# Kernel tuning notes

Measured on AMD Instinct MI355X. Metric: run time of the kernel, lower is better.

Reference implementation:

```python
import jax, jax.numpy as jnp
import numpy as np

B, K, L = 8, 288, 16384   # K = C*kh*kw = 32*3*3
O = 64                    # output channels


def setup_inputs() -> dict:
    key = jax.random.key(0)
    k1, k2, k3 = jax.random.split(key, 3)
    x_unf = jax.random.normal(k1, (B, K, L), dtype=jnp.float32)
    w = jax.random.normal(k2, (O, 32, 3, 3), dtype=jnp.float32)
    b = jax.random.normal(k3, (O,), dtype=jnp.float32)
    gamma = jnp.float32(0.005)
    return {"x_unf": x_unf, "w": w, "b": b, "gamma": gamma}


def reference(x_unf, w, b, gamma):
    # torch: l = x_unf.transpose(1,2)[:,:,:,None] - w.view(1,1,-1,w.size(0))
    #        l = sum(l**2, dim=2); t = exp(-gamma*l) + b
    o = w.shape[0]
    wv = jnp.reshape(w, (-1,))            # row-major flatten, same as torch .view
    wv = jnp.reshape(wv, (-1, o))         # [K, O] (memory reinterpretation, NOT transpose)
    xt = jnp.transpose(x_unf, (0, 2, 1))  # [B, L, K]
    x2 = jnp.sum(xt * xt, axis=-1, keepdims=True)       # [B, L, 1]
    w2 = jnp.sum(wv * wv, axis=0)[None, None, :]        # [1, 1, O]
    xw = jnp.einsum('blk,ko->blo', xt, wv)              # [B, L, O]
    d2 = x2 + w2 - 2.0 * xw                             # [B, L, O]
    t = jnp.exp(-gamma * d2)
    return t + b
```

## Files before the change

kernel.cpp:

```cpp
#include <hip/hip_runtime.h>

#define LDIM 16384
#define KDIM 288
#define ODIM 64
#define BDIM 8

typedef float f32x4 __attribute__((ext_vector_type(4)));
typedef short bf16x8 __attribute__((ext_vector_type(8)));

__device__ __forceinline__ short f2bf(float f) {
  unsigned u = __builtin_bit_cast(unsigned, f);
  unsigned r = u + 0x7FFFu + ((u >> 16) & 1u);
  return (short)(r >> 16);
}

__global__ __launch_bounds__(256) void gauss_pre(const float* __restrict__ w,
                                                 const float* __restrict__ gammap,
                                                 short* __restrict__ wfrag,
                                                 float* __restrict__ cw) {
  int tid = threadIdx.x;
  int blk = blockIdx.x;

  if (blk < 9) {
    int kc = blk;
    int ln = tid & 63;
    int nt = tid >> 6;
    int k0 = kc * 32 + (ln >> 4) * 8;
    int n = nt * 16 + (ln & 15);
    bf16x8 v;
#pragma unroll
    for (int j = 0; j < 8; ++j) v[j] = f2bf(w[(k0 + j) * 64 + n]);
    *(bf16x8*)(wfrag + ((kc * 4 + nt) * 64 + ln) * 8) = v;
  } else {
    __shared__ float red[256];
    int o = tid & 63;
    int seg = tid >> 6;
    float s = 0.f;
#pragma unroll 8
    for (int k = seg * 72; k < seg * 72 + 72; ++k) {
      float v = w[k * 64 + o];
      s += v * v;
    }
    red[tid] = s;
    __syncthreads();
    if (tid < 64) {
      float t = red[tid] + red[tid + 64] + red[tid + 128] + red[tid + 192];
      cw[tid] = -gammap[0] * t;
    }
  }
}

__global__ __launch_bounds__(256, 4) void gauss_main(
    const float* __restrict__ x, const short* __restrict__ wfrag,
    const float* __restrict__ cw, const float* __restrict__ bias,
    const float* __restrict__ gammap, float* __restrict__ out) {
  __shared__ float abuf[2][32 * 128];

  const int tid = threadIdx.x;
  const int lane = tid & 63;
  const int wvid = tid >> 6;
  const int m = lane & 15;
  const int quad = lane >> 4;

  const long g0 = (long)blockIdx.x * 128;
  const int bidx = (int)(g0 >> 14);
  const int l0 = (int)(g0 & (LDIM - 1));

  const float* xb = x + (long)bidx * ((long)KDIM * LDIM) + l0;

  const int srow = (lane >> 5);
  const int scolf = (lane & 31) * 4;

#define STAGE(KC, BUF)                                                         \
  {                                                                            \
    const float* xsrc = xb + (long)((KC) * 32) * LDIM;                         \
    _Pragma("unroll") for (int i = 0; i < 4; ++i) {                            \
      int s = wvid * 4 + i;                                                    \
      const float* gp = xsrc + (long)(2 * s + srow) * LDIM + scolf;            \
      __builtin_amdgcn_global_load_lds(                                        \
          (const __attribute__((address_space(1))) unsigned int*)(void*)gp,    \
          (__attribute__((address_space(3))) unsigned int*)&abuf[BUF][s * 256],\
          16, 0, 0);                                                           \
    }                                                                          \
  }

  const f32x4 zero = {0.f, 0.f, 0.f, 0.f};
  f32x4 acc[2][4];
#pragma unroll
  for (int t = 0; t < 2; ++t)
#pragma unroll
    for (int nt = 0; nt < 4; ++nt) acc[t][nt] = zero;
  float s2[2] = {0.f, 0.f};

  STAGE(0, 0)
  STAGE(1, 1)
  __syncthreads();

#pragma unroll 1
  for (int kc = 0; kc < 9; ++kc) {
    const int pb = kc & 1;

    bf16x8 bfr[4];
    const short* wp = wfrag + ((kc * 4) * 64 + lane) * 8;
#pragma unroll
    for (int nt = 0; nt < 4; ++nt) bfr[nt] = *(const bf16x8*)(wp + nt * 512);

#pragma unroll
    for (int t = 0; t < 2; ++t) {
      const float* ap = &abuf[pb][(quad * 8) * 128 + wvid * 32 + t * 16 + m];
      float a[8];
#pragma unroll
      for (int j = 0; j < 8; ++j) a[j] = ap[j * 128];
      bf16x8 afr;
#pragma unroll
      for (int j = 0; j < 8; ++j) {
        s2[t] += a[j] * a[j];
        afr[j] = f2bf(a[j]);
      }
#pragma unroll
      for (int nt = 0; nt < 4; ++nt)
        acc[t][nt] =
            __builtin_amdgcn_mfma_f32_16x16x32_bf16(afr, bfr[nt], acc[t][nt], 0, 0, 0);
    }

    __syncthreads();
    if (kc < 7) STAGE(kc + 2, pb)
  }

#pragma unroll
  for (int t = 0; t < 2; ++t) {
    s2[t] += __shfl_xor(s2[t], 16, 64);
    s2[t] += __shfl_xor(s2[t], 32, 64);
  }

  const float gamma = gammap[0];
  float cwv[4], bv[4];
#pragma unroll
  for (int nt = 0; nt < 4; ++nt) {
    int col = nt * 16 + m;
    cwv[nt] = cw[col];
    bv[nt] = bias[col];
  }

  float* ob = &abuf[0][0] + wvid * 2048;
  const float coef = 2.f * gamma;
#pragma unroll
  for (int t = 0; t < 2; ++t) {
#pragma unroll
    for (int r = 0; r < 4; ++r) {
      int row = quad * 4 + r;
      float x2v = __shfl(s2[t], (lane & 48) | row, 64);
      float cx = -gamma * x2v;
      int lr = t * 16 + row;
#pragma unroll
      for (int nt = 0; nt < 4; ++nt) {
        float e = coef * acc[t][nt][r] + (cx + cwv[nt]);
        ob[lr * 64 + nt * 16 + m] = __expf(e) + bv[nt];
      }
    }
  }
  __syncthreads();

  float* outw = out + (g0 + wvid * 32) * 64;
#pragma unroll
  for (int j = 0; j < 8; ++j) {
    f32x4 v = *(f32x4*)&ob[j * 256 + lane * 4];
    *(f32x4*)(outw + (j * 4 + (lane >> 4)) * 64 + (lane & 15) * 4) = v;
  }
}

extern "C" void kernel_launch(void* const* d_in, const int* in_sizes, int n_in,
                              void* d_out, int out_size, void* d_ws, size_t ws_size,
                              hipStream_t stream) {
  const float* x = (const float*)d_in[0];
  const float* w = (const float*)d_in[1];
  const float* b = (const float*)d_in[2];
  const float* gamma = (const float*)d_in[3];
  float* out = (float*)d_out;

  short* wfrag = (short*)d_ws;
  float* cw = (float*)((char*)d_ws + 36864);

  gauss_pre<<<10, 256, 0, stream>>>(w, gamma, wfrag, cw);
  gauss_main<<<1024, 256, 0, stream>>>(x, wfrag, cw, b, gamma, out);
}
```

Baseline: 230.0 us.

## Split bf16 hi/lo MFMA for precision, per-wave triple-buffered staging without barriers

Splits both x and w into bf16 high and low parts and runs three MFMAs per tile (hi*hi, lo*hi, hi*lo), recovering near-fp32 accuracy for the dot product. The LDS staging is restructured so each wave loads only its own 32 columns into a private triple buffer. It syncs with vmcnt waits instead of block-wide __syncthreads, and weight fragments are prefetched one chunk ahead. This removes barrier stalls but triples MFMA work, adds register pressure, and lowers the occupancy bound from 4 to 3.

```diff
diff --git a/kernel.cpp b/kernel.cpp
--- a/kernel.cpp
+++ b/kernel.cpp
@@ -13,10 +13,17 @@
   unsigned r = u + 0x7FFFu + ((u >> 16) & 1u);
   return (short)(r >> 16);
 }
+__device__ __forceinline__ float bf2f(short s) {
+  unsigned u = ((unsigned)(unsigned short)s) << 16;
+  return __builtin_bit_cast(float, u);
+}
+
+#define WAITCNT_VM4 0x0F74
 
 __global__ __launch_bounds__(256) void gauss_pre(const float* __restrict__ w,
                                                  const float* __restrict__ gammap,
-                                                 short* __restrict__ wfrag,
+                                                 short* __restrict__ wfh,
+                                                 short* __restrict__ wfl,
                                                  float* __restrict__ cw) {
   int tid = threadIdx.x;
   int blk = blockIdx.x;
@@ -27,10 +34,17 @@
     int nt = tid >> 6;
     int k0 = kc * 32 + (ln >> 4) * 8;
     int n = nt * 16 + (ln & 15);
-    bf16x8 v;
-#pragma unroll
-    for (int j = 0; j < 8; ++j) v[j] = f2bf(w[(k0 + j) * 64 + n]);
-    *(bf16x8*)(wfrag + ((kc * 4 + nt) * 64 + ln) * 8) = v;
+    bf16x8 vh, vl;
+#pragma unroll
+    for (int j = 0; j < 8; ++j) {
+      float v = w[(k0 + j) * 64 + n];
+      short h = f2bf(v);
+      vh[j] = h;
+      vl[j] = f2bf(v - bf2f(h));
+    }
+    int idx = ((kc * 4 + nt) * 64 + ln) * 8;
+    *(bf16x8*)(wfh + idx) = vh;
+    *(bf16x8*)(wfl + idx) = vl;
   } else {
     __shared__ float red[256];
     int o = tid & 63;
@@ -50,11 +64,12 @@
   }
 }
 
-__global__ __launch_bounds__(256, 4) void gauss_main(
-    const float* __restrict__ x, const short* __restrict__ wfrag,
-    const float* __restrict__ cw, const float* __restrict__ bias,
-    const float* __restrict__ gammap, float* __restrict__ out) {
-  __shared__ float abuf[2][32 * 128];
+__global__ __launch_bounds__(256, 3) void gauss_main(
+    const float* __restrict__ x, const short* __restrict__ wfh,
+    const short* __restrict__ wfl, const float* __restrict__ cw,
+    const float* __restrict__ bias, const float* __restrict__ gammap,
+    float* __restrict__ out) {
+  __shared__ float abuf[4][3][1024];
 
   const int tid = threadIdx.x;
   const int lane = tid & 63;
@@ -66,20 +81,19 @@
   const int bidx = (int)(g0 >> 14);
   const int l0 = (int)(g0 & (LDIM - 1));
 
-  const float* xb = x + (long)bidx * ((long)KDIM * LDIM) + l0;
-
-  const int srow = (lane >> 5);
-  const int scolf = (lane & 31) * 4;
-
-#define STAGE(KC, BUF)                                                         \
+  const float* xw = x + (long)bidx * ((long)KDIM * LDIM) + (l0 + wvid * 32);
+  const int strow = lane >> 3;
+  const int stcol = (lane & 7) * 4;
+
+#define STAGE(KC)                                                              \
   {                                                                            \
-    const float* xsrc = xb + (long)((KC) * 32) * LDIM;                         \
+    const float* xsrc = xw + (long)((KC) * 32 + strow) * LDIM + stcol;         \
+    float* lbase = &abuf[wvid][(KC) % 3][0];                                   \
     _Pragma("unroll") for (int i = 0; i < 4; ++i) {                            \
-      int s = wvid * 4 + i;                                                    \
-      const float* gp = xsrc + (long)(2 * s + srow) * LDIM + scolf;            \
       __builtin_amdgcn_global_load_lds(                                        \
-          (const __attribute__((address_space(1))) unsigned int*)(void*)gp,    \
-          (__attribute__((address_space(3))) unsigned int*)&abuf[BUF][s * 256],\
+          (const __attribute__((address_space(1))) unsigned int*)(void*)       \
+              (xsrc + (long)(8 * i) * LDIM),                                   \
+          (__attribute__((address_space(3))) unsigned int*)(lbase + i * 256),  \
           16, 0, 0);                                                           \
     }                                                                          \
   }
@@ -92,39 +106,65 @@
     for (int nt = 0; nt < 4; ++nt) acc[t][nt] = zero;
   float s2[2] = {0.f, 0.f};
 
-  STAGE(0, 0)
-  STAGE(1, 1)
-  __syncthreads();
-
-#pragma unroll 1
+  bf16x8 bh[2][4], bl[2][4];
+
+  STAGE(0)
+  {
+    const short* wp = wfh + (0 * 4 * 64 + lane) * 8;
+    const short* wq = wfl + (0 * 4 * 64 + lane) * 8;
+#pragma unroll
+    for (int nt = 0; nt < 4; ++nt) {
+      bh[0][nt] = *(const bf16x8*)(wp + nt * 512);
+      bl[0][nt] = *(const bf16x8*)(wq + nt * 512);
+    }
+  }
+  STAGE(1)
+
+#pragma unroll
   for (int kc = 0; kc < 9; ++kc) {
-    const int pb = kc & 1;
-
-    bf16x8 bfr[4];
-    const short* wp = wfrag + ((kc * 4) * 64 + lane) * 8;
-#pragma unroll
-    for (int nt = 0; nt < 4; ++nt) bfr[nt] = *(const bf16x8*)(wp + nt * 512);
+    const int cur = kc & 1, nxt = cur ^ 1;
+
+    __builtin_amdgcn_s_waitcnt(WAITCNT_VM4);
+
+    const float* ab = &abuf[wvid][kc % 3][0];
+    float a[2][8];
+#pragma unroll
+    for (int t = 0; t < 2; ++t)
+#pragma unroll
+      for (int j = 0; j < 8; ++j) a[t][j] = ab[(quad * 8 + j) * 32 + t * 16 + m];
+
+    if (kc < 8) {
+      const short* wp = wfh + ((kc + 1) * 4 * 64 + lane) * 8;
+      const short* wq = wfl + ((kc + 1) * 4 * 64 + lane) * 8;
+#pragma unroll
+      for (int nt = 0; nt < 4; ++nt) {
+        bh[nxt][nt] = *(const bf16x8*)(wp + nt * 512);
+        bl[nxt][nt] = *(const bf16x8*)(wq + nt * 512);
+      }
+    }
+    if (kc < 7) STAGE(kc + 2)
 
 #pragma unroll
     for (int t = 0; t < 2; ++t) {
-      const float* ap = &abuf[pb][(quad * 8) * 128 + wvid * 32 + t * 16 + m];
-      float a[8];
-#pragma unroll
-      for (int j = 0; j < 8; ++j) a[j] = ap[j * 128];
-      bf16x8 afr;
+      bf16x8 ah, al;
 #pragma unroll
       for (int j = 0; j < 8; ++j) {
-        s2[t] += a[j] * a[j];
-        afr[j] = f2bf(a[j]);
-      }
-#pragma unroll
-      for (int nt = 0; nt < 4; ++nt)
-        acc[t][nt] =
-            __builtin_amdgcn_mfma_f32_16x16x32_bf16(afr, bfr[nt], acc[t][nt], 0, 0, 0);
-    }
-
-    __syncthreads();
-    if (kc < 7) STAGE(kc + 2, pb)
+        float v = a[t][j];
+        s2[t] += v * v;
+        short h = f2bf(v);
+        ah[j] = h;
+        al[j] = f2bf(v - bf2f(h));
+      }
+#pragma unroll
+      for (int nt = 0; nt < 4; ++nt) {
+        acc[t][nt] = __builtin_amdgcn_mfma_f32_16x16x32_bf16(ah, bh[cur][nt],
+                                                             acc[t][nt], 0, 0, 0);
+        acc[t][nt] = __builtin_amdgcn_mfma_f32_16x16x32_bf16(al, bh[cur][nt],
+                                                             acc[t][nt], 0, 0, 0);
+        acc[t][nt] = __builtin_amdgcn_mfma_f32_16x16x32_bf16(ah, bl[cur][nt],
+                                                             acc[t][nt], 0, 0, 0);
+      }
+    }
   }
 
 #pragma unroll
@@ -142,7 +182,7 @@
     bv[nt] = bias[col];
   }
 
-  float* ob = &abuf[0][0] + wvid * 2048;
+  float* ob = &abuf[wvid][0][0];
   const float coef = 2.f * gamma;
 #pragma unroll
   for (int t = 0; t < 2; ++t) {
@@ -154,12 +194,11 @@
       int lr = t * 16 + row;
 #pragma unroll
       for (int nt = 0; nt < 4; ++nt) {
-        float e = coef * acc[t][nt][r] + (cx + cwv[nt]);
+        float e = __builtin_fmaf(coef, acc[t][nt][r], cx + cwv[nt]);
         ob[lr * 64 + nt * 16 + m] = __expf(e) + bv[nt];
       }
     }
   }
-  __syncthreads();
 
   float* outw = out + (g0 + wvid * 32) * 64;
 #pragma unroll
@@ -178,9 +217,10 @@
   const float* gamma = (const float*)d_in[3];
   float* out = (float*)d_out;
 
-  short* wfrag = (short*)d_ws;
-  float* cw = (float*)((char*)d_ws + 36864);
-
-  gauss_pre<<<10, 256, 0, stream>>>(w, gamma, wfrag, cw);
-  gauss_main<<<1024, 256, 0, stream>>>(x, wfrag, cw, b, gamma, out);
-}
+  short* wfh = (short*)d_ws;
+  short* wfl = (short*)((char*)d_ws + 36864);
+  float* cw = (float*)((char*)d_ws + 73728);
+
+  gauss_pre<<<10, 256, 0, stream>>>(w, gamma, wfh, wfl, cw);
+  gauss_main<<<1024, 256, 0, stream>>>(x, wfh, wfl, cw, b, gamma, out);
+}
```

New measurement: 263.3 us. 14.4% more time.

## Double tile width to 256 rows, switch to fp16 MFMA, prefetch weights

Applied to the files above, without the earlier changes.

Each block now handles 256 L positions instead of 128, with four M-tiles per wave, halving the grid to 512 blocks and doubling LDS per block. The bf16 conversion with manual rounding is replaced by a native fp16 cast and the fp16 MFMA. The pipeline becomes a one-ahead double buffer that prefetches both the next x chunk and the next weight fragments before computing the current one, and the K loop is fully unrolled. This cuts per-element conversion cost and block overhead, at the price of higher register and LDS use, lower occupancy (launch bounds of 2), and fp16 range limits on the inputs.

```diff
diff --git a/kernel.cpp b/kernel.cpp
--- a/kernel.cpp
+++ b/kernel.cpp
@@ -6,17 +6,11 @@
 #define BDIM 8
 
 typedef float f32x4 __attribute__((ext_vector_type(4)));
-typedef short bf16x8 __attribute__((ext_vector_type(8)));
-
-__device__ __forceinline__ short f2bf(float f) {
-  unsigned u = __builtin_bit_cast(unsigned, f);
-  unsigned r = u + 0x7FFFu + ((u >> 16) & 1u);
-  return (short)(r >> 16);
-}
+typedef _Float16 f16x8 __attribute__((ext_vector_type(8)));
 
 __global__ __launch_bounds__(256) void gauss_pre(const float* __restrict__ w,
                                                  const float* __restrict__ gammap,
-                                                 short* __restrict__ wfrag,
+                                                 _Float16* __restrict__ wf,
                                                  float* __restrict__ cw) {
   int tid = threadIdx.x;
   int blk = blockIdx.x;
@@ -27,10 +21,10 @@
     int nt = tid >> 6;
     int k0 = kc * 32 + (ln >> 4) * 8;
     int n = nt * 16 + (ln & 15);
-    bf16x8 v;
+    f16x8 v;
 #pragma unroll
-    for (int j = 0; j < 8; ++j) v[j] = f2bf(w[(k0 + j) * 64 + n]);
-    *(bf16x8*)(wfrag + ((kc * 4 + nt) * 64 + ln) * 8) = v;
+    for (int j = 0; j < 8; ++j) v[j] = (_Float16)w[(k0 + j) * 64 + n];
+    *(f16x8*)(wf + ((kc * 4 + nt) * 64 + ln) * 8) = v;
   } else {
     __shared__ float red[256];
     int o = tid & 63;
@@ -50,11 +44,11 @@
   }
 }
 
-__global__ __launch_bounds__(256, 4) void gauss_main(
-    const float* __restrict__ x, const short* __restrict__ wfrag,
+__global__ __launch_bounds__(256, 2) void gauss_main(
+    const float* __restrict__ x, const _Float16* __restrict__ wf,
     const float* __restrict__ cw, const float* __restrict__ bias,
     const float* __restrict__ gammap, float* __restrict__ out) {
-  __shared__ float abuf[2][32 * 128];
+  __shared__ float abuf[2][32 * 256];
 
   const int tid = threadIdx.x;
   const int lane = tid & 63;
@@ -62,73 +56,78 @@
   const int m = lane & 15;
   const int quad = lane >> 4;
 
-  const long g0 = (long)blockIdx.x * 128;
+  const long g0 = (long)blockIdx.x * 256;
   const int bidx = (int)(g0 >> 14);
   const int l0 = (int)(g0 & (LDIM - 1));
 
   const float* xb = x + (long)bidx * ((long)KDIM * LDIM) + l0;
 
-  const int srow = (lane >> 5);
-  const int scolf = (lane & 31) * 4;
-
 #define STAGE(KC, BUF)                                                         \
   {                                                                            \
-    const float* xsrc = xb + (long)((KC) * 32) * LDIM;                         \
-    _Pragma("unroll") for (int i = 0; i < 4; ++i) {                            \
-      int s = wvid * 4 + i;                                                    \
-      const float* gp = xsrc + (long)(2 * s + srow) * LDIM + scolf;            \
+    const float* xsrc = xb + (long)((KC) * 32 + wvid * 8) * LDIM + lane * 4;   \
+    float* lb = &abuf[BUF][(wvid * 8) * 256];                                  \
+    _Pragma("unroll") for (int i = 0; i < 8; ++i) {                            \
       __builtin_amdgcn_global_load_lds(                                        \
-          (const __attribute__((address_space(1))) unsigned int*)(void*)gp,    \
-          (__attribute__((address_space(3))) unsigned int*)&abuf[BUF][s * 256],\
+          (const __attribute__((address_space(1))) unsigned int*)(void*)       \
+              (xsrc + (long)i * LDIM),                                         \
+          (__attribute__((address_space(3))) unsigned int*)(lb + i * 256),     \
           16, 0, 0);                                                           \
     }                                                                          \
   }
 
   const f32x4 zero = {0.f, 0.f, 0.f, 0.f};
-  f32x4 acc[2][4];
+  f32x4 acc[4][4];
 #pragma unroll
-  for (int t = 0; t < 2; ++t)
+  for (int t = 0; t < 4; ++t)
 #pragma unroll
     for (int nt = 0; nt < 4; ++nt) acc[t][nt] = zero;
-  float s2[2] = {0.f, 0.f};
+  float s2[4] = {0.f, 0.f, 0.f, 0.f};
+
+  f16x8 bf[2][4];
 
   STAGE(0, 0)
-  STAGE(1, 1)
+  {
+    const _Float16* wp = wf + (0 * 4 * 64 + lane) * 8;
+#pragma unroll
+    for (int nt = 0; nt < 4; ++nt) bf[0][nt] = *(const f16x8*)(wp + nt * 512);
+  }
   __syncthreads();
 
-#pragma unroll 1
+#pragma unroll
   for (int kc = 0; kc < 9; ++kc) {
     const int pb = kc & 1;
 
-    bf16x8 bfr[4];
-    const short* wp = wfrag + ((kc * 4) * 64 + lane) * 8;
+    if (kc < 8) {
+      STAGE(kc + 1, pb ^ 1)
+      const _Float16* wp = wf + ((kc + 1) * 4 * 64 + lane) * 8;
 #pragma unroll
-    for (int nt = 0; nt < 4; ++nt) bfr[nt] = *(const bf16x8*)(wp + nt * 512);
+      for (int nt = 0; nt < 4; ++nt)
+        bf[pb ^ 1][nt] = *(const f16x8*)(wp + nt * 512);
+    }
 
 #pragma unroll
-    for (int t = 0; t < 2; ++t) {
-      const float* ap = &abuf[pb][(quad * 8) * 128 + wvid * 32 + t * 16 + m];
+    for (int t = 0; t < 4; ++t) {
+      const float* ap = &abuf[pb][(quad * 8) * 256 + wvid * 64 + t * 16 + m];
       float a[8];
 #pragma unroll
-      for (int j = 0; j < 8; ++j) a[j] = ap[j * 128];
-      bf16x8 afr;
+      for (int j = 0; j < 8; ++j) a[j] = ap[j * 256];
+      f16x8 af;
 #pragma unroll
       for (int j = 0; j < 8; ++j) {
         s2[t] += a[j] * a[j];
-        afr[j] = f2bf(a[j]);
+        af[j] = (_Float16)a[j];
       }
 #pragma unroll
       for (int nt = 0; nt < 4; ++nt)
         acc[t][nt] =
-            __builtin_amdgcn_mfma_f32_16x16x32_bf16(afr, bfr[nt], acc[t][nt], 0, 0, 0);
+            __builtin_amdgcn_mfma_f32_16x16x32_f16(af, bf[pb][nt], acc[t][nt], 0, 0, 0);
     }
 
-    __syncthreads();
-    if (kc < 7) STAGE(kc + 2, pb)
+    if (kc < 8) __syncthreads();
   }
 
 #pragma unroll
-  for (int t = 0; t < 2; ++t) {
+  for (int t = 0; t < 4; ++t) {
     s2[t] += __shfl_xor(s2[t], 16, 64);
     s2[t] += __shfl_xor(s2[t], 32, 64);
   }
@@ -142,10 +141,12 @@
     bv[nt] = bias[col];
   }
 
-  float* ob = &abuf[0][0] + wvid * 2048;
+  __syncthreads();
+
+  float* ob = &abuf[0][0] + wvid * 4096;
   const float coef = 2.f * gamma;
 #pragma unroll
-  for (int t = 0; t < 2; ++t) {
+  for (int t = 0; t < 4; ++t) {
 #pragma unroll
     for (int r = 0; r < 4; ++r) {
       int row = quad * 4 + r;
@@ -154,18 +155,17 @@
       int lr = t * 16 + row;
 #pragma unroll
       for (int nt = 0; nt < 4; ++nt) {
-        float e = coef * acc[t][nt][r] + (cx + cwv[nt]);
+        float e = __builtin_fmaf(coef, acc[t][nt][r], cx + cwv[nt]);
         ob[lr * 64 + nt * 16 + m] = __expf(e) + bv[nt];
       }
     }
   }
-  __syncthreads();
 
-  float* outw = out + (g0 + wvid * 32) * 64;
+  float* outw = out + (g0 + wvid * 64) * 64;
 #pragma unroll
-  for (int j = 0; j < 8; ++j) {
+  for (int j = 0; j < 16; ++j) {
     f32x4 v = *(f32x4*)&ob[j * 256 + lane * 4];
-    *(f32x4*)(outw + (j * 4 + (lane >> 4)) * 64 + (lane & 15) * 4) = v;
+    *(f32x4*)(outw + j * 256 + lane * 4) = v;
   }
 }
 
@@ -178,9 +178,9 @@
   const float* gamma = (const float*)d_in[3];
   float* out = (float*)d_out;
 
-  short* wfrag = (short*)d_ws;
+  _Float16* wf = (_Float16*)d_ws;
   float* cw = (float*)((char*)d_ws + 36864);
 
-  gauss_pre<<<10, 256, 0, stream>>>(w, gamma, wfrag, cw);
-  gauss_main<<<1024, 256, 0, stream>>>(x, wfrag, cw, b, gamma, out);
+  gauss_pre<<<10, 256, 0, stream>>>(w, gamma, wf, cw);
+  gauss_main<<<512, 256, 0, stream>>>(x, wf, cw, b, gamma, out);
 }
```

Result: slower. 255.2 us (+10.9%).
